# Optimization experiments

Measured on AMD Instinct MI355X. Metric: run time of the kernel, lower is better.

The kernel has to match this reference:

```python
import jax, jax.numpy as jnp
import numpy as np


def _rotate_matrices(angles):
    # angles: (M, 1) -> rot (M, 2, 2), rows [[c, -s], [s, c]]
    c = jnp.cos(angles)
    s = jnp.sin(angles)
    rot = jnp.stack([jnp.concatenate([c, -s], axis=1),
                     jnp.concatenate([s, c], axis=1)], axis=1)
    return rot, jnp.swapaxes(rot, 1, 2)


def _seq_group_permute(x, mapping, perms, final=False):
    # x: (B, S, d), perms: (d//2, 2, 2)
    B, S, d = x.shape
    if not final:
        x = x[:, :, mapping]
    x = x.reshape(B, S, d // 2, 2)
    x = jnp.einsum('ijmk,mkn->ijmn', x, perms).reshape(B, S, d)
    if final:
        x = x[:, :, mapping]
    return x


def _mat_group_permute_inv(m, mapping, perms_inv, transposed):
    # m: (R, d), perms_inv: (d//2, 2, 2)
    R, d = m.shape
    m = m[:, mapping].reshape(R, d // 2, 2)
    sub = 'imk,mkn->imn' if transposed else 'imk,mnk->imn'
    return jnp.einsum(sub, m, perms_inv).reshape(R, d)


def setup_inputs() -> dict:
    key = jax.random.key(0)
    ks = jax.random.split(key, 8)
    B, S, IN, OUT = 4, 2048, 1024, 4096
    inp = jax.random.normal(ks[0], (B, S, IN), dtype=jnp.float32)
    weight = jax.random.normal(ks[1], (OUT, IN), dtype=jnp.float32) * 0.02
    mask = (jax.random.uniform(ks[2], (OUT, IN)) > 0.5).astype(jnp.float32)
    in_scores = jax.random.normal(ks[3], (IN // 2, 1), dtype=jnp.float32)
    out_scores = jax.random.normal(ks[4], (OUT // 2, 1), dtype=jnp.float32)
    in_mapping = jax.random.permutation(ks[5], IN).astype(jnp.int32)
    out_mapping = jax.random.permutation(ks[6], OUT).astype(jnp.int32)
    out_mapping_reverse = jnp.argsort(out_mapping).astype(jnp.int32)
    return {
        'input': inp,
        'weight': weight,
        'mask': mask,
        'in_permutation_scores': in_scores,
        'out_permutation_scores': out_scores,
        'in_mapping': in_mapping,
        'out_mapping': out_mapping,
        'out_mapping_reverse': out_mapping_reverse,
        'temperature': 1,
    }


def reference(input, weight, mask, in_permutation_scores, out_permutation_scores,
              in_mapping, out_mapping, out_mapping_reverse, temperature):
    in_permut, in_permut_inv = _rotate_matrices(in_permutation_scores)
    out_permut, out_permut_inv = _rotate_matrices(out_permutation_scores)
    # permute + rotate activations on the input side
    s_in = _seq_group_permute(input, in_mapping, in_permut)
    # inverse permute/rotate the weight's input dim, then its output dim
    m2 = _mat_group_permute_inv(weight, in_mapping, in_permut_inv, transposed=False)
    m3 = _mat_group_permute_inv(m2.T, out_mapping, out_permut_inv, transposed=True)
    m3 = m3 * mask.T  # (in, out)
    s_inner = jnp.einsum('bsi,io->bso', s_in, m3)
    s_out = _seq_group_permute(s_inner, out_mapping_reverse, out_permut, final=True)
    return s_out
```

## Files before the change

### kernel.cpp

```cpp
#include <hip/hip_runtime.h>
#include <hip/hip_bf16.h>
#include <stdint.h>

#define M_DIM 8192
#define K_DIM 1024
#define N_DIM 4096

typedef __bf16 bf16x8 __attribute__((ext_vector_type(8)));
typedef float  f32x4  __attribute__((ext_vector_type(4)));

__device__ __forceinline__ uint16_t f2bf(float f) {
  union { float f; uint32_t u; } x; x.f = f;
  uint32_t u = x.u;
  return (uint16_t)((u + 0x7FFFu + ((u >> 16) & 1u)) >> 16);
}

__global__ __launch_bounds__(256) void convert_bf16_kernel(
    const float* __restrict__ in, uint16_t* __restrict__ out, int n4) {
  int i = blockIdx.x * 256 + threadIdx.x;
  if (i >= n4) return;
  float4 v = ((const float4*)in)[i];
  ushort4 o;
  o.x = f2bf(v.x); o.y = f2bf(v.y); o.z = f2bf(v.z); o.w = f2bf(v.w);
  ((ushort4*)out)[i] = o;
}

__global__ __launch_bounds__(256) void build_w_kernel(
    const float* __restrict__ weight,
    const float* __restrict__ mask,
    const float* __restrict__ in_scores,
    const float* __restrict__ out_scores,
    const int*   __restrict__ in_mapping,
    const int*   __restrict__ out_mapping,
    uint16_t*    __restrict__ w5t)
{
  __shared__ float    w0[K_DIM], w1[K_DIM];
  __shared__ uint16_t o0[K_DIM], o1[K_DIM];

  const int mo = blockIdx.x;
  const int t  = threadIdx.x;

  const int r0 = out_mapping[2 * mo];
  const int r1 = out_mapping[2 * mo + 1];

  ((float4*)w0)[t] = ((const float4*)(weight + (size_t)r0 * K_DIM))[t];
  ((float4*)w1)[t] = ((const float4*)(weight + (size_t)r1 * K_DIM))[t];

  const float ao = out_scores[mo];
  const float so = sinf(ao), co = cosf(ao);

  __syncthreads();

#pragma unroll
  for (int s = 0; s < 2; s++) {
    const int mi = t + s * 256;
    const float ai = in_scores[mi];
    const float si = sinf(ai), ci = cosf(ai);
    const int ia0 = in_mapping[2 * mi];
    const int ia1 = in_mapping[2 * mi + 1];

    const float w00 = w0[ia0], w01 = w0[ia1];
    const float w10 = w1[ia0], w11 = w1[ia1];

    float a00 =  ci * w00 + si * w01;
    float a01 = -si * w00 + ci * w01;
    float a10 =  ci * w10 + si * w11;
    float a11 = -si * w10 + ci * w11;

    float b00 = co * a00 - so * a10;
    float b10 = co * a01 - so * a11;
    float b01 = so * a00 + co * a10;
    float b11 = so * a01 + co * a11;

    const float2 mk0 = *(const float2*)&mask[(size_t)(2 * mo) * K_DIM + 2 * mi];
    const float2 mk1 = *(const float2*)&mask[(size_t)(2 * mo + 1) * K_DIM + 2 * mi];
    b00 *= mk0.x; b10 *= mk0.y;
    b01 *= mk1.x; b11 *= mk1.y;

    float c00 =  co * b00 + so * b01;
    float c10 =  co * b10 + so * b11;
    float c01 = -so * b00 + co * b01;
    float c11 = -so * b10 + co * b11;

    o0[ia0] = f2bf(ci * c00 - si * c10);
    o0[ia1] = f2bf(si * c00 + ci * c10);
    o1[ia0] = f2bf(ci * c01 - si * c11);
    o1[ia1] = f2bf(si * c01 + ci * c11);
  }

  __syncthreads();

  ((uint2*)(w5t + (size_t)r0 * K_DIM))[t] = ((const uint2*)o0)[t];
  ((uint2*)(w5t + (size_t)r1 * K_DIM))[t] = ((const uint2*)o1)[t];
}


__device__ __forceinline__ void async_load16(const uint16_t* g, uint16_t* lds_wave_uniform) {
  __builtin_amdgcn_global_load_lds(
      (const __attribute__((address_space(1))) uint32_t*)g,
      (__attribute__((address_space(3))) uint32_t*)lds_wave_uniform,
      16, 0, 0);
}

__global__ __launch_bounds__(256, 2) void gemm_kernel(
    const uint16_t* __restrict__ A,
    const uint16_t* __restrict__ BT,
    float* __restrict__ C)
{
  __shared__ __align__(16) uint16_t As[128 * 64];
  __shared__ __align__(16) uint16_t Bs[128 * 64];

  const int tid  = threadIdx.x;
  const int wave = tid >> 6;
  const int lane = tid & 63;
  const int quad = lane >> 4;
  const int rr   = lane & 15;
  const int bn   = blockIdx.x;
  const int bm   = blockIdx.y;
  const int wm   = (wave >> 1) * 64;
  const int wn   = (wave & 1) * 64;

  f32x4 acc[4][4] = {};

  const uint16_t* gA[4];
  const uint16_t* gB[4];
  uint16_t* lA[4];
  uint16_t* lB[4];
#pragma unroll
  for (int it = 0; it < 4; it++) {
    const int c   = it * 256 + tid;
    const int row = c >> 3;
    const int h   = c & 7;
    const int g   = h ^ (row & 7);
    gA[it] = A  + (size_t)(bm * 128 + row) * K_DIM + g * 8;
    gB[it] = BT + (size_t)(bn * 128 + row) * K_DIM + g * 8;
    lA[it] = &As[(it * 256 + wave * 64) * 8];
    lB[it] = &Bs[(it * 256 + wave * 64) * 8];
  }

  for (int k0 = 0; k0 < K_DIM; k0 += 64) {
#pragma unroll
    for (int it = 0; it < 4; it++) {
      async_load16(gA[it] + k0, lA[it]);
      async_load16(gB[it] + k0, lB[it]);
    }
    __syncthreads();

    bf16x8 af[4][2], bfr[4][2];
#pragma unroll
    for (int i = 0; i < 4; i++) {
      const int r = wm + i * 16 + rr;
#pragma unroll
      for (int s = 0; s < 2; s++) {
        const int gk = s * 4 + quad;
        af[i][s] = *reinterpret_cast<const bf16x8*>(&As[(r * 8 + (gk ^ (r & 7))) * 8]);
      }
    }
#pragma unroll
    for (int j = 0; j < 4; j++) {
      const int r = wn + j * 16 + rr;
#pragma unroll
      for (int s = 0; s < 2; s++) {
        const int gk = s * 4 + quad;
        bfr[j][s] = *reinterpret_cast<const bf16x8*>(&Bs[(r * 8 + (gk ^ (r & 7))) * 8]);
      }
    }

#pragma unroll
    for (int s = 0; s < 2; s++)
#pragma unroll
      for (int i = 0; i < 4; i++)
#pragma unroll
        for (int j = 0; j < 4; j++)
          acc[i][j] = __builtin_amdgcn_mfma_f32_16x16x32_bf16(af[i][s], bfr[j][s], acc[i][j], 0, 0, 0);

    __syncthreads();
  }

#pragma unroll
  for (int i = 0; i < 4; i++) {
#pragma unroll
    for (int j = 0; j < 4; j++) {
      const int colg = bn * 128 + wn + j * 16 + rr;
#pragma unroll
      for (int rg = 0; rg < 4; rg++) {
        const int rowg = bm * 128 + wm + i * 16 + quad * 4 + rg;
        C[(size_t)rowg * N_DIM + colg] = acc[i][j][rg];
      }
    }
  }
}

extern "C" void kernel_launch(void* const* d_in, const int* in_sizes, int n_in,
                              void* d_out, int out_size, void* d_ws, size_t ws_size,
                              hipStream_t stream) {
  const float* input      = (const float*)d_in[0];
  const float* weight     = (const float*)d_in[1];
  const float* mask       = (const float*)d_in[2];
  const float* in_scores  = (const float*)d_in[3];
  const float* out_scores = (const float*)d_in[4];
  const int*   in_mapping = (const int*)d_in[5];
  const int*   out_mapping= (const int*)d_in[6];
  float* out = (float*)d_out;

  uint16_t* a_bf16 = (uint16_t*)d_ws;
  uint16_t* w5t    = (uint16_t*)d_ws + (size_t)M_DIM * K_DIM;

  convert_bf16_kernel<<<(M_DIM * K_DIM / 4 + 255) / 256, 256, 0, stream>>>(
      input, a_bf16, M_DIM * K_DIM / 4);

  build_w_kernel<<<2048, 256, 0, stream>>>(
      weight, mask, in_scores, out_scores, in_mapping, out_mapping, w5t);

  dim3 grid(N_DIM / 128, M_DIM / 128);
  gemm_kernel<<<grid, 256, 0, stream>>>(a_bf16, w5t, out);
}
```

Measured before the change: 256.4 us.

## Triple-buffer GEMM with async prefetch, 256x128 tiles, and block swizzle

The GEMM kernel moves to 512-thread blocks computing 256x128 output tiles, and uses a three-slot LDS ring in which tile k+2 is prefetched while tile k is computed. Partial vmcnt waits replace full syncs. A grid swizzle groups blocks for L2 reuse, and s_setprio raises priority around the MFMA bursts. The aim is to hide global-load latency and cut barrier stalls, at the cost of 144KB of LDS per block, which lowers occupancy.

```diff
diff --git a/kernel.cpp b/kernel.cpp
--- a/kernel.cpp
+++ b/kernel.cpp
@@ -102,90 +102,142 @@
       16, 0, 0);
 }
 
-__global__ __launch_bounds__(256, 2) void gemm_kernel(
+template <int VM>
+__device__ __forceinline__ void wait_vm() {
+  if constexpr (VM == 12)     asm volatile("s_waitcnt vmcnt(12)" ::: "memory");
+  else if constexpr (VM == 6) asm volatile("s_waitcnt vmcnt(6)"  ::: "memory");
+  else                        asm volatile("s_waitcnt vmcnt(0)"  ::: "memory");
+}
+
+__global__ __launch_bounds__(512, 2) void gemm_kernel(
     const uint16_t* __restrict__ A,
     const uint16_t* __restrict__ BT,
     float* __restrict__ C)
 {
-  __shared__ __align__(16) uint16_t As[128 * 64];
-  __shared__ __align__(16) uint16_t Bs[128 * 64];
+  __shared__ __align__(16) uint16_t As[3][256 * 64];
+  __shared__ __align__(16) uint16_t Bs[3][128 * 64];
 
   const int tid  = threadIdx.x;
-  const int wave = tid >> 6;
+  const int w    = tid >> 6;
   const int lane = tid & 63;
   const int quad = lane >> 4;
   const int rr   = lane & 15;
-  const int bn   = blockIdx.x;
-  const int bm   = blockIdx.y;
-  const int wm   = (wave >> 1) * 64;
-  const int wn   = (wave & 1) * 64;
+  const int wm   = w >> 1;
+  const int wn   = w & 1;
+
+  const int flat = blockIdx.y * gridDim.x + blockIdx.x;
+  const int swz  = ((flat & 7) << 7) | (flat >> 3);
+  const int bm   = swz >> 5;
+  const int bn   = swz & 31;
 
   f32x4 acc[4][4] = {};
 
   const uint16_t* gA[4];
-  const uint16_t* gB[4];
-  uint16_t* lA[4];
-  uint16_t* lB[4];
-#pragma unroll
-  for (int it = 0; it < 4; it++) {
-    const int c   = it * 256 + tid;
+  const uint16_t* gB[2];
+#pragma unroll
+  for (int ii = 0; ii < 4; ii++) {
+    const int c   = ii * 512 + tid;
     const int row = c >> 3;
-    const int h   = c & 7;
-    const int g   = h ^ (row & 7);
-    gA[it] = A  + (size_t)(bm * 128 + row) * K_DIM + g * 8;
-    gB[it] = BT + (size_t)(bn * 128 + row) * K_DIM + g * 8;
-    lA[it] = &As[(it * 256 + wave * 64) * 8];
-    lB[it] = &Bs[(it * 256 + wave * 64) * 8];
-  }
-
-  for (int k0 = 0; k0 < K_DIM; k0 += 64) {
-#pragma unroll
-    for (int it = 0; it < 4; it++) {
-      async_load16(gA[it] + k0, lA[it]);
-      async_load16(gB[it] + k0, lB[it]);
+    const int g   = (c & 7) ^ (row & 7);
+    gA[ii] = A + (size_t)(bm * 256 + row) * K_DIM + g * 8;
+  }
+#pragma unroll
+  for (int ii = 0; ii < 2; ii++) {
+    const int c   = ii * 512 + tid;
+    const int row = c >> 3;
+    const int g   = (c & 7) ^ (row & 7);
+    gB[ii] = BT + (size_t)(bn * 128 + row) * K_DIM + g * 8;
+  }
+
+  int offA[4][2], offB[4][2];
+#pragma unroll
+  for (int i = 0; i < 4; i++) {
+    const int r = wm * 64 + i * 16 + rr;
+#pragma unroll
+    for (int kh = 0; kh < 2; kh++) {
+      const int gk = kh * 4 + quad;
+      offA[i][kh] = (r * 8 + (gk ^ (r & 7))) * 8;
     }
-    __syncthreads();
-
-    bf16x8 af[4][2], bfr[4][2];
-#pragma unroll
-    for (int i = 0; i < 4; i++) {
-      const int r = wm + i * 16 + rr;
-#pragma unroll
-      for (int s = 0; s < 2; s++) {
-        const int gk = s * 4 + quad;
-        af[i][s] = *reinterpret_cast<const bf16x8*>(&As[(r * 8 + (gk ^ (r & 7))) * 8]);
-      }
+  }
+#pragma unroll
+  for (int j = 0; j < 4; j++) {
+    const int r = wn * 64 + j * 16 + rr;
+#pragma unroll
+    for (int kh = 0; kh < 2; kh++) {
+      const int gk = kh * 4 + quad;
+      offB[j][kh] = (r * 8 + (gk ^ (r & 7))) * 8;
     }
+  }
+
+#define STAGE(TIDX, SLOT)                                                     \
+  do {                                                                        \
+    const int k0s_ = (TIDX) * 64;                                             \
+    _Pragma("unroll")                                                         \
+    for (int ii_ = 0; ii_ < 4; ii_++)                                         \
+      async_load16(gA[ii_] + k0s_, &As[SLOT][(ii_ * 512 + w * 64) * 8]);      \
+    _Pragma("unroll")                                                         \
+    for (int ii_ = 0; ii_ < 2; ii_++)                                         \
+      async_load16(gB[ii_] + k0s_, &Bs[SLOT][(ii_ * 512 + w * 64) * 8]);      \
+  } while (0)
+
+#define TILE_BODY(VM, SLOT)                                                   \
+  do {                                                                        \
+    wait_vm<VM>();                         \
+    __builtin_amdgcn_s_barrier();          \
+    __builtin_amdgcn_sched_barrier(0);     \
+    const uint16_t* as_ = &As[SLOT][0];                                       \
+    const uint16_t* bs_ = &Bs[SLOT][0];                                       \
+    bf16x8 af[4][2], bfv[4][2];                                               \
+    _Pragma("unroll")                                                         \
+    for (int i_ = 0; i_ < 4; i_++)                                            \
+      _Pragma("unroll")                                                       \
+      for (int kh_ = 0; kh_ < 2; kh_++)                                       \
+        af[i_][kh_] = *reinterpret_cast<const bf16x8*>(as_ + offA[i_][kh_]);  \
+    _Pragma("unroll")                                                         \
+    for (int j_ = 0; j_ < 4; j_++)                                            \
+      _Pragma("unroll")                                                       \
+      for (int kh_ = 0; kh_ < 2; kh_++)                                       \
+        bfv[j_][kh_] = *reinterpret_cast<const bf16x8*>(bs_ + offB[j_][kh_]); \
+    __builtin_amdgcn_s_setprio(1);                                            \
+    _Pragma("unroll")                                                         \
+    for (int kh_ = 0; kh_ < 2; kh_++)                                         \
+      _Pragma("unroll")                                                       \
+      for (int i_ = 0; i_ < 4; i_++)                                          \
+        _Pragma("unroll")                                                     \
+        for (int j_ = 0; j_ < 4; j_++)                                        \
+          acc[i_][j_] = __builtin_amdgcn_mfma_f32_16x16x32_bf16(              \
+              af[i_][kh_], bfv[j_][kh_], acc[i_][j_], 0, 0, 0);               \
+    __builtin_amdgcn_s_setprio(0);                                            \
+    __builtin_amdgcn_s_barrier();          \
+  } while (0)
+
+  STAGE(0, 0);
+  STAGE(1, 1);
+
+  int sc = 0;
+  int sn = 2;
+  for (int t = 0; t < 14; ++t) {
+    STAGE(t + 2, sn);
+    TILE_BODY(12, sc);
+    sc = (sc == 2) ? 0 : sc + 1;
+    sn = (sn == 2) ? 0 : sn + 1;
+  }
+  TILE_BODY(6, sc);
+  sc = (sc == 2) ? 0 : sc + 1;
+  TILE_BODY(0, sc);
+
+#undef STAGE
+#undef TILE_BODY
+
+#pragma unroll
+  for (int i = 0; i < 4; i++) {
+    const int row0 = bm * 256 + wm * 64 + i * 16 + quad * 4;
 #pragma unroll
     for (int j = 0; j < 4; j++) {
-      const int r = wn + j * 16 + rr;
-#pragma unroll
-      for (int s = 0; s < 2; s++) {
-        const int gk = s * 4 + quad;
-        bfr[j][s] = *reinterpret_cast<const bf16x8*>(&Bs[(r * 8 + (gk ^ (r & 7))) * 8]);
-      }
-    }
-
-#pragma unroll
-    for (int s = 0; s < 2; s++)
-#pragma unroll
-      for (int i = 0; i < 4; i++)
-#pragma unroll
-        for (int j = 0; j < 4; j++)
-          acc[i][j] = __builtin_amdgcn_mfma_f32_16x16x32_bf16(af[i][s], bfr[j][s], acc[i][j], 0, 0, 0);
-
-    __syncthreads();
-  }
-
-#pragma unroll
-  for (int i = 0; i < 4; i++) {
-#pragma unroll
-    for (int j = 0; j < 4; j++) {
-      const int colg = bn * 128 + wn + j * 16 + rr;
+      const int col = bn * 128 + wn * 64 + j * 16 + rr;
 #pragma unroll
       for (int rg = 0; rg < 4; rg++) {
-        const int rowg = bm * 128 + wm + i * 16 + quad * 4 + rg;
-        C[(size_t)rowg * N_DIM + colg] = acc[i][j][rg];
+        C[(size_t)(row0 + rg) * N_DIM + col] = acc[i][j][rg];
       }
     }
   }
@@ -212,6 +264,6 @@
   build_w_kernel<<<2048, 256, 0, stream>>>(
       weight, mask, in_scores, out_scores, in_mapping, out_mapping, w5t);
 
-  dim3 grid(N_DIM / 128, M_DIM / 128);
-  gemm_kernel<<<grid, 256, 0, stream>>>(a_bf16, w5t, out);
-}
+  dim3 grid(32, 32);
+  gemm_kernel<<<grid, 512, 0, stream>>>(a_bf16, w5t, out);
+}
```

Measured after the change: 278.4 us. 1.09x slower.

## Restructure GEMM into 256x256 tiles with double-buffered async LDS pipeline

Applied to the files above, without the earlier changes.

The GEMM moves from 128x128 tiles on 256 threads to 256x256 tiles on 512 threads (8 waves, each owning 128x64). The K loop is software-pipelined with double-buffered LDS: A and B half-tiles are prefetched one and two steps ahead while MFMAs run. Explicit barriers, waitcnt, setprio and sched_barrier pin the interleaving. A block-index swizzle improves L2 locality. In exchange it uses 128 KB of LDS and more accumulator registers, which lowers occupancy and makes correctness depend on the hand-counted vmcnt values.

```diff
diff --git a/kernel.cpp b/kernel.cpp
--- a/kernel.cpp
+++ b/kernel.cpp
@@ -102,90 +102,148 @@
       16, 0, 0);
 }
 
-__global__ __launch_bounds__(256, 2) void gemm_kernel(
+__global__ __launch_bounds__(512, 2) void gemm_kernel(
     const uint16_t* __restrict__ A,
     const uint16_t* __restrict__ BT,
     float* __restrict__ C)
 {
-  __shared__ __align__(16) uint16_t As[128 * 64];
-  __shared__ __align__(16) uint16_t Bs[128 * 64];
+  __shared__ __align__(16) uint16_t As[2][2][128 * 64];
+  __shared__ __align__(16) uint16_t Bs[2][2][128 * 64];
 
   const int tid  = threadIdx.x;
-  const int wave = tid >> 6;
+  const int w    = tid >> 6;
   const int lane = tid & 63;
   const int quad = lane >> 4;
   const int rr   = lane & 15;
-  const int bn   = blockIdx.x;
-  const int bm   = blockIdx.y;
-  const int wm   = (wave >> 1) * 64;
-  const int wn   = (wave & 1) * 64;
-
-  f32x4 acc[4][4] = {};
-
-  const uint16_t* gA[4];
-  const uint16_t* gB[4];
-  uint16_t* lA[4];
-  uint16_t* lB[4];
-#pragma unroll
-  for (int it = 0; it < 4; it++) {
-    const int c   = it * 256 + tid;
+  const int wm   = w >> 2;
+  const int wn   = w & 3;
+  const int hA   = wm;
+  const int hB   = wn >> 1;
+
+  const int flat = blockIdx.y * gridDim.x + blockIdx.x;
+  const int swz  = ((flat & 7) << 6) | (flat >> 3);
+  const int bm   = swz >> 4;
+  const int bn   = swz & 15;
+
+  f32x4 acc[8][4] = {};
+
+  const uint16_t* gA[2];
+  const uint16_t* gB[2];
+#pragma unroll
+  for (int ii = 0; ii < 2; ii++) {
+    const int c   = ii * 512 + tid;
     const int row = c >> 3;
-    const int h   = c & 7;
-    const int g   = h ^ (row & 7);
-    gA[it] = A  + (size_t)(bm * 128 + row) * K_DIM + g * 8;
-    gB[it] = BT + (size_t)(bn * 128 + row) * K_DIM + g * 8;
-    lA[it] = &As[(it * 256 + wave * 64) * 8];
-    lB[it] = &Bs[(it * 256 + wave * 64) * 8];
-  }
-
-  for (int k0 = 0; k0 < K_DIM; k0 += 64) {
-#pragma unroll
-    for (int it = 0; it < 4; it++) {
-      async_load16(gA[it] + k0, lA[it]);
-      async_load16(gB[it] + k0, lB[it]);
+    const int g   = (c & 7) ^ (row & 7);
+    gA[ii] = A  + (size_t)(bm * 256 + row) * K_DIM + g * 8;
+    gB[ii] = BT + (size_t)(bn * 256 + row) * K_DIM + g * 8;
+  }
+
+#define STAGE_A(BUF, H, KT)                                                   \
+  do {                                                                        \
+    _Pragma("unroll")                                                         \
+    for (int ii_ = 0; ii_ < 2; ii_++)                                         \
+      async_load16(gA[ii_] + (H) * (128 * K_DIM) + (KT) * 64,                 \
+                   &As[BUF][H][(ii_ * 512 + w * 64) * 8]);                    \
+  } while (0)
+
+#define STAGE_B(BUF, H, KT)                                                   \
+  do {                                                                        \
+    _Pragma("unroll")                                                         \
+    for (int ii_ = 0; ii_ < 2; ii_++)                                         \
+      async_load16(gB[ii_] + (H) * (128 * K_DIM) + (KT) * 64,                 \
+                   &Bs[BUF][H][(ii_ * 512 + w * 64) * 8]);                    \
+  } while (0)
+
+  int offA[8][2], offB[4][2];
+#pragma unroll
+  for (int i = 0; i < 8; i++) {
+    const int r = i * 16 + rr;
+#pragma unroll
+    for (int s = 0; s < 2; s++) {
+      const int gk = s * 4 + quad;
+      offA[i][s] = (r * 8 + (gk ^ (r & 7))) * 8;
     }
-    __syncthreads();
-
-    bf16x8 af[4][2], bfr[4][2];
-#pragma unroll
-    for (int i = 0; i < 4; i++) {
-      const int r = wm + i * 16 + rr;
-#pragma unroll
-      for (int s = 0; s < 2; s++) {
-        const int gk = s * 4 + quad;
-        af[i][s] = *reinterpret_cast<const bf16x8*>(&As[(r * 8 + (gk ^ (r & 7))) * 8]);
-      }
+  }
+#pragma unroll
+  for (int j = 0; j < 4; j++) {
+    const int r = (wn & 1) * 64 + j * 16 + rr;
+#pragma unroll
+    for (int s = 0; s < 2; s++) {
+      const int gk = s * 4 + quad;
+      offB[j][s] = (r * 8 + (gk ^ (r & 7))) * 8;
     }
+  }
+
+#define PHASE(P, STAGE_STMT, WAIT_STMT)                                        \
+  {                                                                            \
+    bf16x8 af[2][2];                                                           \
+    _Pragma("unroll")                                                          \
+    for (int d_ = 0; d_ < 2; d_++)                                             \
+      _Pragma("unroll")                                                        \
+      for (int s_ = 0; s_ < 2; s_++)                                           \
+        af[d_][s_] = *reinterpret_cast<const bf16x8*>(asb + offA[2*(P)+d_][s_]); \
+    STAGE_STMT;                                                                \
+    WAIT_STMT;                                                                 \
+    __builtin_amdgcn_sched_barrier(0);                                         \
+    __builtin_amdgcn_s_barrier();                                              \
+    asm volatile("s_waitcnt lgkmcnt(0)" ::: "memory");                         \
+    __builtin_amdgcn_sched_barrier(0);                                         \
+    __builtin_amdgcn_s_setprio(1);                                             \
+    _Pragma("unroll")                                                          \
+    for (int s_ = 0; s_ < 2; s_++)                                             \
+      _Pragma("unroll")                                                        \
+      for (int d_ = 0; d_ < 2; d_++)                                           \
+        _Pragma("unroll")                                                      \
+        for (int j_ = 0; j_ < 4; j_++)                                         \
+          acc[2*(P)+d_][j_] = __builtin_amdgcn_mfma_f32_16x16x32_bf16(         \
+              af[d_][s_], bfv[j_][s_], acc[2*(P)+d_][j_], 0, 0, 0);            \
+    __builtin_amdgcn_s_setprio(0);                                             \
+    __builtin_amdgcn_sched_barrier(0);                                         \
+    __builtin_amdgcn_s_barrier();                                              \
+    __builtin_amdgcn_sched_barrier(0);                                         \
+  }
+
+  STAGE_B(0, 0, 0); STAGE_B(0, 1, 0);
+  STAGE_A(0, 0, 0); STAGE_A(0, 1, 0);
+  STAGE_B(1, 0, 1); STAGE_B(1, 1, 1);
+  asm volatile("s_waitcnt vmcnt(4)" ::: "memory");
+  __builtin_amdgcn_s_barrier();
+  __builtin_amdgcn_sched_barrier(0);
+
+  for (int t = 0; t < 16; ++t) {
+    const int buf  = t & 1;
+    const int nbuf = buf ^ 1;
+    const uint16_t* asb = &As[buf][hA][0];
+    const uint16_t* bsb = &Bs[buf][hB][0];
+
+    bf16x8 bfv[4][2];
+#pragma unroll
+    for (int j = 0; j < 4; j++)
+#pragma unroll
+      for (int s = 0; s < 2; s++)
+        bfv[j][s] = *reinterpret_cast<const bf16x8*>(bsb + offB[j][s]);
+
+    PHASE(0, { if (t < 15) STAGE_A(nbuf, 0, t + 1); }, {});
+    PHASE(1, { if (t < 15) STAGE_A(nbuf, 1, t + 1); }, {});
+    PHASE(2, { if (t < 14) STAGE_B(buf, 0, t + 2); }, {});
+    PHASE(3, { if (t < 14) STAGE_B(buf, 1, t + 2); },
+          { if (t < 14)       { asm volatile("s_waitcnt vmcnt(4)" ::: "memory"); }
+            else if (t == 14) { asm volatile("s_waitcnt vmcnt(0)" ::: "memory"); } });
+  }
+
+#undef PHASE
+#undef STAGE_A
+#undef STAGE_B
+
+#pragma unroll
+  for (int i = 0; i < 8; i++) {
+    const int row0 = bm * 256 + wm * 128 + i * 16 + quad * 4;
 #pragma unroll
     for (int j = 0; j < 4; j++) {
-      const int r = wn + j * 16 + rr;
-#pragma unroll
-      for (int s = 0; s < 2; s++) {
-        const int gk = s * 4 + quad;
-        bfr[j][s] = *reinterpret_cast<const bf16x8*>(&Bs[(r * 8 + (gk ^ (r & 7))) * 8]);
-      }
-    }
-
-#pragma unroll
-    for (int s = 0; s < 2; s++)
-#pragma unroll
-      for (int i = 0; i < 4; i++)
-#pragma unroll
-        for (int j = 0; j < 4; j++)
-          acc[i][j] = __builtin_amdgcn_mfma_f32_16x16x32_bf16(af[i][s], bfr[j][s], acc[i][j], 0, 0, 0);
-
-    __syncthreads();
-  }
-
-#pragma unroll
-  for (int i = 0; i < 4; i++) {
-#pragma unroll
-    for (int j = 0; j < 4; j++) {
-      const int colg = bn * 128 + wn + j * 16 + rr;
+      const int col = bn * 256 + wn * 64 + j * 16 + rr;
 #pragma unroll
       for (int rg = 0; rg < 4; rg++) {
-        const int rowg = bm * 128 + wm + i * 16 + quad * 4 + rg;
-        C[(size_t)rowg * N_DIM + colg] = acc[i][j][rg];
+        C[(size_t)(row0 + rg) * N_DIM + col] = acc[i][j][rg];
       }
     }
   }
@@ -212,6 +270,6 @@
   build_w_kernel<<<2048, 256, 0, stream>>>(
       weight, mask, in_scores, out_scores, in_mapping, out_mapping, w5t);
 
-  dim3 grid(N_DIM / 128, M_DIM / 128);
-  gemm_kernel<<<grid, 256, 0, stream>>>(a_bf16, w5t, out);
-}
+  dim3 grid(N_DIM / 256, M_DIM / 256);
+  gemm_kernel<<<grid, 512, 0, stream>>>(a_bf16, w5t, out);
+}
```

After: 260.9 us. No clear change (+1.8%).

## Double-buffer GEMM with 256x128 tiles, swizzled grid, and fused prologue kernels

Applied to the files above, without the earlier changes.

Merges the input bf16 conversion and the weight-building kernel into one launch, with extra blocks doing the conversion. The GEMM moves to a 256x128 block tile with BK=32 and double-buffered LDS. The next K-tile is prefetched while MFMAs run, using explicit waitcnt and barriers plus s_setprio. A 1D grid with an XCD-aware swizzle improves L2 locality. Risks are higher register pressure (acc[8][4]) and fewer blocks (1024), which may lower occupancy.

```diff
diff --git a/kernel.cpp b/kernel.cpp
--- a/kernel.cpp
+++ b/kernel.cpp
@@ -15,30 +15,33 @@
   return (uint16_t)((u + 0x7FFFu + ((u >> 16) & 1u)) >> 16);
 }
 
-__global__ __launch_bounds__(256) void convert_bf16_kernel(
-    const float* __restrict__ in, uint16_t* __restrict__ out, int n4) {
-  int i = blockIdx.x * 256 + threadIdx.x;
-  if (i >= n4) return;
-  float4 v = ((const float4*)in)[i];
-  ushort4 o;
-  o.x = f2bf(v.x); o.y = f2bf(v.y); o.z = f2bf(v.z); o.w = f2bf(v.w);
-  ((ushort4*)out)[i] = o;
-}
-
-__global__ __launch_bounds__(256) void build_w_kernel(
+__global__ __launch_bounds__(256) void prologue_kernel(
+    const float* __restrict__ input,
     const float* __restrict__ weight,
     const float* __restrict__ mask,
     const float* __restrict__ in_scores,
     const float* __restrict__ out_scores,
     const int*   __restrict__ in_mapping,
     const int*   __restrict__ out_mapping,
+    uint16_t*    __restrict__ a_bf16,
     uint16_t*    __restrict__ w5t)
 {
   __shared__ float    w0[K_DIM], w1[K_DIM];
   __shared__ uint16_t o0[K_DIM], o1[K_DIM];
 
-  const int mo = blockIdx.x;
-  const int t  = threadIdx.x;
+  const int bid = blockIdx.x;
+  const int t   = threadIdx.x;
+
+  if (bid >= 2048) {
+    const int i = (bid - 2048) * 256 + t;
+    float4 v = ((const float4*)input)[i];
+    ushort4 o;
+    o.x = f2bf(v.x); o.y = f2bf(v.y); o.z = f2bf(v.z); o.w = f2bf(v.w);
+    ((ushort4*)a_bf16)[i] = o;
+    return;
+  }
+
+  const int mo = bid;
 
   const int r0 = out_mapping[2 * mo];
   const int r1 = out_mapping[2 * mo + 1];
@@ -94,7 +97,6 @@
   ((uint2*)(w5t + (size_t)r1 * K_DIM))[t] = ((const uint2*)o1)[t];
 }
 
-
 __device__ __forceinline__ void async_load16(const uint16_t* g, uint16_t* lds_wave_uniform) {
   __builtin_amdgcn_global_load_lds(
       (const __attribute__((address_space(1))) uint32_t*)g,
@@ -107,85 +109,111 @@
     const uint16_t* __restrict__ BT,
     float* __restrict__ C)
 {
-  __shared__ __align__(16) uint16_t As[128 * 64];
-  __shared__ __align__(16) uint16_t Bs[128 * 64];
+  __shared__ __align__(16) uint16_t As[2][256 * 32];
+  __shared__ __align__(16) uint16_t Bs[2][128 * 32];
 
   const int tid  = threadIdx.x;
-  const int wave = tid >> 6;
+  const int w    = tid >> 6;
   const int lane = tid & 63;
   const int quad = lane >> 4;
   const int rr   = lane & 15;
-  const int bn   = blockIdx.x;
-  const int bm   = blockIdx.y;
-  const int wm   = (wave >> 1) * 64;
-  const int wn   = (wave & 1) * 64;
-
-  f32x4 acc[4][4] = {};
+  const int wm2  = w >> 1;
+  const int wn2  = w & 1;
+
+  const int flat = blockIdx.x;
+  const int swz  = ((flat & 7) << 7) | (flat >> 3);
+  const int bm   = swz >> 5;
+  const int bn   = swz & 31;
+
+  f32x4 acc[8][4] = {};
 
   const uint16_t* gA[4];
-  const uint16_t* gB[4];
-  uint16_t* lA[4];
-  uint16_t* lB[4];
-#pragma unroll
-  for (int it = 0; it < 4; it++) {
-    const int c   = it * 256 + tid;
-    const int row = c >> 3;
-    const int h   = c & 7;
-    const int g   = h ^ (row & 7);
-    gA[it] = A  + (size_t)(bm * 128 + row) * K_DIM + g * 8;
-    gB[it] = BT + (size_t)(bn * 128 + row) * K_DIM + g * 8;
-    lA[it] = &As[(it * 256 + wave * 64) * 8];
-    lB[it] = &Bs[(it * 256 + wave * 64) * 8];
-  }
-
-  for (int k0 = 0; k0 < K_DIM; k0 += 64) {
-#pragma unroll
-    for (int it = 0; it < 4; it++) {
-      async_load16(gA[it] + k0, lA[it]);
-      async_load16(gB[it] + k0, lB[it]);
-    }
-    __syncthreads();
-
-    bf16x8 af[4][2], bfr[4][2];
-#pragma unroll
-    for (int i = 0; i < 4; i++) {
-      const int r = wm + i * 16 + rr;
-#pragma unroll
-      for (int s = 0; s < 2; s++) {
-        const int gk = s * 4 + quad;
-        af[i][s] = *reinterpret_cast<const bf16x8*>(&As[(r * 8 + (gk ^ (r & 7))) * 8]);
-      }
-    }
+  const uint16_t* gB[2];
+#pragma unroll
+  for (int ii = 0; ii < 4; ii++) {
+    const int c   = ii * 256 + tid;
+    const int row = c >> 2;
+    const int g   = (c & 3) ^ ((row >> 1) & 3);
+    gA[ii] = A + (size_t)(bm * 256 + row) * K_DIM + g * 8;
+  }
+#pragma unroll
+  for (int ii = 0; ii < 2; ii++) {
+    const int c   = ii * 256 + tid;
+    const int row = c >> 2;
+    const int g   = (c & 3) ^ ((row >> 1) & 3);
+    gB[ii] = BT + (size_t)(bn * 128 + row) * K_DIM + g * 8;
+  }
+
+#define STAGE(BUF, KT)                                                        \
+  do {                                                                        \
+    _Pragma("unroll")                                                         \
+    for (int ii_ = 0; ii_ < 4; ii_++)                                         \
+      async_load16(gA[ii_] + (KT) * 32, &As[BUF][(ii_ * 256 + w * 64) * 8]);  \
+    _Pragma("unroll")                                                         \
+    for (int ii_ = 0; ii_ < 2; ii_++)                                         \
+      async_load16(gB[ii_] + (KT) * 32, &Bs[BUF][(ii_ * 256 + w * 64) * 8]);  \
+  } while (0)
+
+  int offA[8], offB[4];
+#pragma unroll
+  for (int i = 0; i < 8; i++) {
+    const int r = wm2 * 128 + i * 16 + rr;
+    offA[i] = (r * 4 + (quad ^ ((r >> 1) & 3))) * 8;
+  }
+#pragma unroll
+  for (int j = 0; j < 4; j++) {
+    const int r = wn2 * 64 + j * 16 + rr;
+    offB[j] = (r * 4 + (quad ^ ((r >> 1) & 3))) * 8;
+  }
+
+#define TILE(T, MODE)                                                         \
+  {                                                                           \
+    const int buf_ = (T) & 1;                                                 \
+    const uint16_t* asb_ = &As[buf_][0];                                      \
+    const uint16_t* bsb_ = &Bs[buf_][0];                                      \
+    bf16x8 af[8], bf[4];                                                      \
+    _Pragma("unroll") for (int i_ = 0; i_ < 8; i_++)                          \
+      af[i_] = *reinterpret_cast<const bf16x8*>(asb_ + offA[i_]);             \
+    _Pragma("unroll") for (int j_ = 0; j_ < 4; j_++)                          \
+      bf[j_] = *reinterpret_cast<const bf16x8*>(bsb_ + offB[j_]);             \
+    asm volatile("s_waitcnt lgkmcnt(0)" ::: "memory");                        \
+    __builtin_amdgcn_sched_barrier(0);      \
+    __builtin_amdgcn_s_barrier();            \
+    if (MODE == 0) STAGE(buf_, (T) + 2);                                      \
+    __builtin_amdgcn_s_setprio(1);                                            \
+    _Pragma("unroll") for (int i_ = 0; i_ < 8; i_++)                          \
+      _Pragma("unroll") for (int j_ = 0; j_ < 4; j_++)                        \
+        acc[i_][j_] = __builtin_amdgcn_mfma_f32_16x16x32_bf16(                \
+            af[i_], bf[j_], acc[i_][j_], 0, 0, 0);                            \
+    __builtin_amdgcn_s_setprio(0);                                            \
+    if (MODE == 0)      { asm volatile("s_waitcnt vmcnt(6)" ::: "memory"); }  \
+    else if (MODE == 1) { asm volatile("s_waitcnt vmcnt(0)" ::: "memory"); }  \
+    if (MODE < 2) __builtin_amdgcn_s_barrier();                               \
+  }
+
+  STAGE(0, 0);
+  STAGE(1, 1);
+  asm volatile("s_waitcnt vmcnt(6)" ::: "memory");
+  __builtin_amdgcn_s_barrier();
+
+  for (int t = 0; t < 30; ++t) {
+    TILE(t, 0);
+  }
+  TILE(30, 1);
+  TILE(31, 2);
+
+#undef TILE
+#undef STAGE
+
+#pragma unroll
+  for (int i = 0; i < 8; i++) {
+    const int row0 = bm * 256 + wm2 * 128 + i * 16 + quad * 4;
 #pragma unroll
     for (int j = 0; j < 4; j++) {
-      const int r = wn + j * 16 + rr;
-#pragma unroll
-      for (int s = 0; s < 2; s++) {
-        const int gk = s * 4 + quad;
-        bfr[j][s] = *reinterpret_cast<const bf16x8*>(&Bs[(r * 8 + (gk ^ (r & 7))) * 8]);
-      }
-    }
-
-#pragma unroll
-    for (int s = 0; s < 2; s++)
-#pragma unroll
-      for (int i = 0; i < 4; i++)
-#pragma unroll
-        for (int j = 0; j < 4; j++)
-          acc[i][j] = __builtin_amdgcn_mfma_f32_16x16x32_bf16(af[i][s], bfr[j][s], acc[i][j], 0, 0, 0);
-
-    __syncthreads();
-  }
-
-#pragma unroll
-  for (int i = 0; i < 4; i++) {
-#pragma unroll
-    for (int j = 0; j < 4; j++) {
-      const int colg = bn * 128 + wn + j * 16 + rr;
+      const int col = bn * 128 + wn2 * 64 + j * 16 + rr;
 #pragma unroll
       for (int rg = 0; rg < 4; rg++) {
-        const int rowg = bm * 128 + wm + i * 16 + quad * 4 + rg;
-        C[(size_t)rowg * N_DIM + colg] = acc[i][j][rg];
+        C[(size_t)(row0 + rg) * N_DIM + col] = acc[i][j][rg];
       }
     }
   }
@@ -206,12 +234,9 @@
   uint16_t* a_bf16 = (uint16_t*)d_ws;
   uint16_t* w5t    = (uint16_t*)d_ws + (size_t)M_DIM * K_DIM;
 
-  convert_bf16_kernel<<<(M_DIM * K_DIM / 4 + 255) / 256, 256, 0, stream>>>(
-      input, a_bf16, M_DIM * K_DIM / 4);
-
-  build_w_kernel<<<2048, 256, 0, stream>>>(
-      weight, mask, in_scores, out_scores, in_mapping, out_mapping, w5t);
-
-  dim3 grid(N_DIM / 128, M_DIM / 128);
-  gemm_kernel<<<grid, 256, 0, stream>>>(a_bf16, w5t, out);
-}
+  prologue_kernel<<<10240, 256, 0, stream>>>(
+      input, weight, mask, in_scores, out_scores, in_mapping, out_mapping,
+      a_bf16, w5t);
+
+  gemm_kernel<<<1024, 256, 0, stream>>>(a_bf16, w5t, out);
+}
```

Result: no change. 254.3 us (-0.8%).
